# Performance work log

Hardware: AMD Instinct MI355X
Metric: run time of the kernel (lower is better)

Reference implementation:

```python
import jax, jax.numpy as jnp
import numpy as np

N, E, T = 6144, 98304, 32
D_IN, D, D_FF, H, OUT = 128, 256, 256, 4, 2
DH = D // H
EPS = 1e-5


def setup_inputs() -> dict:
    key = jax.random.key(0)
    ks = jax.random.split(key, 24)
    s = 0.05
    inp = {
        "x": jax.random.normal(ks[0], (N, D_IN), jnp.float32),
        "edge_index": jax.random.randint(ks[1], (2, E), 0, N, jnp.int64 if jax.config.jax_enable_x64 else jnp.int32),
        "timesteps": jnp.sort(jax.random.randint(ks[2], (N,), 0, T)),
        "lin_l_w": jax.random.normal(ks[3], (D, D_IN), jnp.float32) * s,
        "lin_l_b": jnp.zeros((D,), jnp.float32),
        "lin_r_w": jax.random.normal(ks[4], (D, D_IN), jnp.float32) * s,
        "bn_gamma": jnp.ones((D,), jnp.float32),
        "bn_beta": jnp.zeros((D,), jnp.float32),
        "in_proj_w": jax.random.normal(ks[5], (2, 3 * D, D), jnp.float32) * s,
        "in_proj_b": jnp.zeros((2, 3 * D), jnp.float32),
        "out_w": jax.random.normal(ks[6], (2, D, D), jnp.float32) * s,
        "out_b": jnp.zeros((2, D), jnp.float32),
        "ff1_w": jax.random.normal(ks[7], (2, D_FF, D), jnp.float32) * s,
        "ff1_b": jnp.zeros((2, D_FF), jnp.float32),
        "ff2_w": jax.random.normal(ks[8], (2, D, D_FF), jnp.float32) * s,
        "ff2_b": jnp.zeros((2, D), jnp.float32),
        "ln1_g": jnp.ones((2, D), jnp.float32),
        "ln1_b": jnp.zeros((2, D), jnp.float32),
        "ln2_g": jnp.ones((2, D), jnp.float32),
        "ln2_b": jnp.zeros((2, D), jnp.float32),
        "cls_w": jax.random.normal(ks[9], (OUT, D), jnp.float32) * s,
        "cls_b": jnp.zeros((OUT,), jnp.float32),
    }
    return inp


def _layernorm(h, g, b):
    mu = jnp.mean(h, -1, keepdims=True)
    v = jnp.var(h, -1, keepdims=True)
    return (h - mu) * jax.lax.rsqrt(v + EPS) * g + b


def _forward(x, edge_index, timesteps, lin_l_w, lin_l_b, lin_r_w, bn_gamma, bn_beta,
             in_proj_w, in_proj_b, out_w, out_b, ff1_w, ff1_b, ff2_w, ff2_b,
             ln1_g, ln1_b, ln2_g, ln2_b, cls_w, cls_b):
    # SAGEConv (mean aggregation): out = lin_l(mean_{j->i} x_j) + lin_r(x_i)
    src, dst = edge_index[0], edge_index[1]
    agg = jax.ops.segment_sum(x[src], dst, num_segments=N)
    cnt = jax.ops.segment_sum(jnp.ones((E,), x.dtype), dst, num_segments=N)
    agg = agg / jnp.maximum(cnt, 1.0)[:, None]
    h = agg @ lin_l_w.T + lin_l_b + x @ lin_r_w.T

    # BatchNorm1d (training batch stats) + ReLU
    mu = jnp.mean(h, 0)
    var = jnp.var(h, 0)
    h = (h - mu) * jax.lax.rsqrt(var + EPS) * bn_gamma + bn_beta
    h = jax.nn.relu(h)

    # Per-timestep transformer == full attention with block-diagonal mask
    mask = timesteps[:, None] == timesteps[None, :]  # [N, N]
    neg = jnp.finfo(h.dtype).min

    for l in range(2):
        # self-attention (post-norm TransformerEncoderLayer)
        qkv = h @ in_proj_w[l].T + in_proj_b[l]             # [N, 3D]
        q, k, v = jnp.split(qkv, 3, axis=-1)
        q = q.reshape(N, H, DH).transpose(1, 0, 2)          # [H, N, DH]
        k = k.reshape(N, H, DH).transpose(1, 0, 2)
        v = v.reshape(N, H, DH).transpose(1, 0, 2)
        scores = jnp.einsum('hnd,hmd->hnm', q, k) / jnp.sqrt(jnp.asarray(DH, h.dtype))
        scores = jnp.where(mask[None], scores, neg)
        attn = jax.nn.softmax(scores, axis=-1)
        o = jnp.einsum('hnm,hmd->hnd', attn, v).transpose(1, 0, 2).reshape(N, D)
        o = o @ out_w[l].T + out_b[l]
        h = _layernorm(h + o, ln1_g[l], ln1_b[l])
        # FFN
        f = jax.nn.relu(h @ ff1_w[l].T + ff1_b[l]) @ ff2_w[l].T + ff2_b[l]
        h = _layernorm(h + f, ln2_g[l], ln2_b[l])

    return h @ cls_w.T + cls_b  # [N, OUT]


def reference(x, edge_index, timesteps, lin_l_w, lin_l_b, lin_r_w, bn_gamma, bn_beta,
              in_proj_w, in_proj_b, out_w, out_b, ff1_w, ff1_b, ff2_w, ff2_b,
              ln1_g, ln1_b, ln2_g, ln2_b, cls_w, cls_b):
    return _forward(x, edge_index, timesteps, lin_l_w, lin_l_b, lin_r_w, bn_gamma, bn_beta,
                    in_proj_w, in_proj_b, out_w, out_b, ff1_w, ff1_b, ff2_w, ff2_b,
                    ln1_g, ln1_b, ln2_g, ln2_b, cls_w, cls_b)
```

## Files before the change

### kernel.cpp

```cpp
#include <hip/hip_runtime.h>

#define NN   6144
#define EE   98304
#define DIN  128
#define DD   256
#define TT   32
#define NH   4
#define ATTN_Z 6
#define WROWS 3328

typedef __attribute__((ext_vector_type(8))) short short8;
typedef __attribute__((ext_vector_type(4))) float f32x4;
typedef unsigned short u16;

__device__ __forceinline__ float bf2f(u16 u) {
    return __uint_as_float(((unsigned)u) << 16);
}
__device__ __forceinline__ u16 f2bf(float f) {
    unsigned u = __float_as_uint(f);
    return (u16)((u + 0x7fffu + ((u >> 16) & 1u)) >> 16);
}
__device__ __forceinline__ unsigned pk2(float a, float b) {
    return (unsigned)f2bf(a) | ((unsigned)f2bf(b) << 16);
}
__device__ __forceinline__ float bnrelu(float v, float s, float q, float g, float b) {
    float mu = s * (1.0f / NN);
    float var = q * (1.0f / NN) - mu * mu;
    return fmaxf((v - mu) * rsqrtf(var + 1e-5f) * g + b, 0.0f);
}

__global__ void aml_hist_k(const int* __restrict__ ei, int* __restrict__ deg) {
    int e = blockIdx.x * 256 + threadIdx.x;
    if (e < EE) atomicAdd(&deg[ei[EE + e]], 1);
}

__global__ void aml_scan_k(const int* __restrict__ deg, int* __restrict__ rowptr,
                           int* __restrict__ cursor) {
    int t = threadIdx.x;
    int base = t * 24;
    int loc[24];
    int s = 0;
    #pragma unroll
    for (int j = 0; j < 24; ++j) { loc[j] = s; s += deg[base + j]; }
    __shared__ int part[256];
    part[t] = s;
    __syncthreads();
    for (int o = 1; o < 256; o <<= 1) {
        int v = (t >= o) ? part[t - o] : 0;
        __syncthreads();
        part[t] += v;
        __syncthreads();
    }
    int off = (t > 0) ? part[t - 1] : 0;
    #pragma unroll
    for (int j = 0; j < 24; ++j) {
        rowptr[base + j] = off + loc[j];
        cursor[base + j] = off + loc[j];
    }
    if (t == 255) rowptr[NN] = part[255];
}

__global__ void aml_scatter2_k(const int* __restrict__ ei, int* __restrict__ cursor,
                               int* __restrict__ eid) {
    int e = blockIdx.x * 256 + threadIdx.x;
    if (e >= EE) return;
    int slot = atomicAdd(&cursor[ei[EE + e]], 1);
    eid[slot] = ei[e];
}

__global__ void aml_gather_k(const float* __restrict__ x, const int* __restrict__ rowptr,
                             const int* __restrict__ eid, u16* __restrict__ ac) {
    int node = blockIdx.x * 4 + (threadIdx.x >> 6);
    int lane = threadIdx.x & 63;
    int p0 = rowptr[node], p1 = rowptr[node + 1];
    float ax = 0.f, ay = 0.f;
    int j = p0;
    for (; j + 1 < p1; j += 2) {
        int s0 = eid[j], s1 = eid[j + 1];
        float2 v0 = *(const float2*)(x + (size_t)s0 * DIN + lane * 2);
        float2 v1 = *(const float2*)(x + (size_t)s1 * DIN + lane * 2);
        ax += v0.x + v1.x; ay += v0.y + v1.y;
    }
    if (j < p1) {
        float2 v = *(const float2*)(x + (size_t)eid[j] * DIN + lane * 2);
        ax += v.x; ay += v.y;
    }
    float inv = 1.0f / fmaxf((float)(p1 - p0), 1.0f);
    float2 xr = *(const float2*)(x + (size_t)node * DIN + lane * 2);
    *(unsigned*)(ac + (size_t)node * DD + lane * 2) = pk2(ax * inv, ay * inv);
    *(unsigned*)(ac + (size_t)node * DD + DIN + lane * 2) = pk2(xr.x, xr.y);
}

__global__ void aml_prep_k(const float* __restrict__ lin_l_w, const float* __restrict__ lin_r_w,
                           const float* __restrict__ inp_w, const float* __restrict__ out_w,
                           const float* __restrict__ ff1_w, const float* __restrict__ ff2_w,
                           const int* __restrict__ ts, u16* __restrict__ wb,
                           int* __restrict__ offs, float* __restrict__ zero_region) {
    int r = blockIdx.x;
    if (r > WROWS) {
        zero_region[(r - WROWS - 1) * 256 + threadIdx.x] = 0.0f;
        return;
    }
    if (r == WROWS) {
        int t = threadIdx.x;
        if (t <= TT) {
            int lo = 0, hi = NN;
            while (lo < hi) { int mid = (lo + hi) >> 1; if (ts[mid] < t) lo = mid + 1; else hi = mid; }
            offs[t] = lo;
        }
        return;
    }
    int k = threadIdx.x;
    float v;
    if (r < 256) {
        v = (k < DIN) ? lin_l_w[r * DIN + k] : lin_r_w[r * DIN + (k - DIN)];
    } else {
        int r2 = r - 256;
        int l = r2 / 1536, r3 = r2 % 1536;
        const float* src; int rr;
        if (r3 < 768)       { src = inp_w + (size_t)l * 768 * DD; rr = r3; }
        else if (r3 < 1024) { src = out_w + (size_t)l * DD * DD;  rr = r3 - 768; }
        else if (r3 < 1280) { src = ff1_w + (size_t)l * DD * DD;  rr = r3 - 1024; }
        else                { src = ff2_w + (size_t)l * DD * DD;  rr = r3 - 1280; }
        v = src[(size_t)rr * DD + k];
    }
    wb[(size_t)r * DD + k] = f2bf(v);
}

template <int RELU, int AMODE, int CF32, int BNSTAT, int CT2>
__global__ __launch_bounds__(256)
void aml_gemm_k(const void* __restrict__ A, const u16* __restrict__ Wb,
                const float* __restrict__ bias, void* __restrict__ C, int M,
                float* __restrict__ stats, const float* __restrict__ bng,
                const float* __restrict__ bnb, float* __restrict__ h2) {
    __shared__ __align__(16) unsigned char lds[65536];
    const int t = threadIdx.x;
    const int brow = blockIdx.x * 64;
    const int bcol = blockIdx.y * (64 * CT2);

    #pragma unroll
    for (int p = 0; p < 8; ++p) {
        int c = t + p * 256;
        int row = c >> 5;
        int colb = (c & 31) * 16;
        int dst = row * 512 + (colb ^ ((row & 7) << 4));
        if (AMODE == 2) {
            int d0 = (c & 31) * 8;
            const u16* sA = (const u16*)A + (size_t)(brow + row) * 256 + d0;
            uint4 raw = *(const uint4*)sA;
            const u16* rp = (const u16*)&raw;
            float av[8];
            #pragma unroll
            for (int i = 0; i < 8; ++i) {
                int d = d0 + i;
                av[i] = bnrelu(bf2f(rp[i]), stats[d], stats[DD + d], bng[d], bnb[d]);
            }
            if (blockIdx.y == 0) {
                float* hp = h2 + (size_t)(brow + row) * 256 + d0;
                *(float4*)hp = make_float4(av[0], av[1], av[2], av[3]);
                *(float4*)(hp + 4) = make_float4(av[4], av[5], av[6], av[7]);
            }
            uint4 pa = { pk2(av[0], av[1]), pk2(av[2], av[3]), pk2(av[4], av[5]), pk2(av[6], av[7]) };
            *(uint4*)(lds + dst) = pa;
        } else {
            const u16* sA = (const u16*)A + (size_t)(brow + row) * 256 + (c & 31) * 8;
            *(uint4*)(lds + dst) = *(const uint4*)sA;
        }
        *(uint4*)(lds + 32768 + dst) =
            *(const uint4*)(Wb + (size_t)(bcol + row) * 256 + (c & 31) * 8);
    }
    __syncthreads();

    const int wave = t >> 6, lane = t & 63;
    const int lrow = lane & 15, lk = lane >> 4;
    const int arow = wave * 16 + lrow;

    short8 af[8];
    #pragma unroll
    for (int ks = 0; ks < 8; ++ks) {
        int kbyte = ks * 64 + lk * 16;
        af[ks] = *(const short8*)(lds + arow * 512 + (kbyte ^ ((arow & 7) << 4)));
    }

    f32x4 acc[CT2][4] = {};
    #pragma unroll
    for (int c2 = 0; c2 < CT2; ++c2) {
        if (c2) {
            __syncthreads();
            #pragma unroll
            for (int p = 0; p < 8; ++p) {
                int c = t + p * 256;
                int row = c >> 5;
                int colb = (c & 31) * 16;
                int dst = 32768 + row * 512 + (colb ^ ((row & 7) << 4));
                *(uint4*)(lds + dst) =
                    *(const uint4*)(Wb + (size_t)(bcol + c2 * 64 + row) * 256 + (c & 31) * 8);
            }
            __syncthreads();
        }
        #pragma unroll
        for (int ks = 0; ks < 8; ++ks) {
            int kbyte = ks * 64 + lk * 16;
            #pragma unroll
            for (int ct = 0; ct < 4; ++ct) {
                int wrow = ct * 16 + lrow;
                short8 bf = *(const short8*)(lds + 32768 + wrow * 512 + (kbyte ^ ((wrow & 7) << 4)));
                acc[c2][ct] = __builtin_amdgcn_mfma_f32_16x16x32_bf16(af[ks], bf, acc[c2][ct], 0, 0, 0);
            }
        }
    }

    #pragma unroll
    for (int c2 = 0; c2 < CT2; ++c2) {
        #pragma unroll
        for (int ct = 0; ct < 4; ++ct) {
            int col = bcol + c2 * 64 + ct * 16 + lrow;
            float bv = bias[col];
            float s = 0.f, q = 0.f;
            #pragma unroll
            for (int r = 0; r < 4; ++r) {
                int grow = brow + wave * 16 + lk * 4 + r;
                float v = acc[c2][ct][r] + bv;
                if (RELU) v = fmaxf(v, 0.0f);
                if (CF32) ((float*)C)[(size_t)grow * M + col] = v;
                else      ((u16*)C)[(size_t)grow * M + col] = f2bf(v);
                if (BNSTAT) { s += v; q += v * v; }
            }
            if (BNSTAT) {
                s += __shfl_xor(s, 16); s += __shfl_xor(s, 32);
                q += __shfl_xor(q, 16); q += __shfl_xor(q, 32);
                if (lk == 0) {
                    atomicAdd(&stats[col], s);
                    atomicAdd(&stats[DD + col], q);
                }
            }
        }
    }
}

#define TAIL_GEMM(WPTR, LOADA)                                                            \
    _Pragma("unroll")                                                                     \
    for (int kc = 0; kc < 4; ++kc) {                                                      \
        __syncthreads();                                                                  \
        _Pragma("unroll")                                                                 \
        for (int p = 0; p < 8; ++p) {                                                     \
            int c = t + p * 256;                                                          \
            int row = c >> 3, sub = c & 7;                                                \
            *(uint4*)(Wl + row * 128 + ((sub * 16) ^ ((row & 7) << 4))) =                 \
                *(const uint4*)((WPTR) + (size_t)row * 256 + kc * 64 + sub * 8);          \
        }                                                                                 \
        __syncthreads();                                                                  \
        if ((LOADA) && kc == 0) {                                                         \
            _Pragma("unroll")                                                             \
            for (int ks = 0; ks < 8; ++ks) {                                              \
                int kbyte = ks * 64 + lk * 16;                                            \
                af[ks] = *(const short8*)(Al + lrow * 512 + (kbyte ^ ((lrow & 7) << 4))); \
            }                                                                             \
        }                                                                                 \
        _Pragma("unroll")                                                                 \
        for (int s = 0; s < 2; ++s) {                                                     \
            int kb = s * 64 + lk * 16;                                                    \
            _Pragma("unroll")                                                             \
            for (int ct = 0; ct < 4; ++ct) {                                              \
                int wrow = wcol + ct * 16 + lrow;                                         \
                short8 bf = *(const short8*)(Wl + wrow * 128 + (kb ^ ((wrow & 7) << 4))); \
                acc[ct] = __builtin_amdgcn_mfma_f32_16x16x32_bf16(af[kc * 2 + s], bf,     \
                                                                  acc[ct], 0, 0, 0);      \
            }                                                                             \
        }                                                                                 \
    }

#define WRITE_AL(VARR)                                                                    \
    _Pragma("unroll")                                                                     \
    for (int ct = 0; ct < 4; ++ct) {                                                      \
        _Pragma("unroll")                                                                 \
        for (int r = 0; r < 4; ++r) {                                                     \
            int row = lk * 4 + r, col = wcol + ct * 16 + lrow;                            \
            *(u16*)(Al + row * 512 + ((col * 2) ^ ((row & 7) << 4))) = f2bf(VARR[ct][r]); \
        }                                                                                 \
    }

#define ROW_LN_STATS(S4, Q4, MU, IV)                                                      \
    _Pragma("unroll")                                                                     \
    for (int off = 1; off < 16; off <<= 1) {                                              \
        _Pragma("unroll")                                                                 \
        for (int r = 0; r < 4; ++r) {                                                     \
            S4[r] += __shfl_xor(S4[r], off);                                              \
            Q4[r] += __shfl_xor(Q4[r], off);                                              \
        }                                                                                 \
    }                                                                                     \
    if (lrow == 0) {                                                                      \
        _Pragma("unroll")                                                                 \
        for (int r = 0; r < 4; ++r) {                                                     \
            reds[wave][lk * 4 + r] = S4[r];                                               \
            redq[wave][lk * 4 + r] = Q4[r];                                               \
        }                                                                                 \
    }                                                                                     \
    __syncthreads();                                                                      \
    _Pragma("unroll")                                                                     \
    for (int r = 0; r < 4; ++r) {                                                         \
        int rr = lk * 4 + r;                                                              \
        float S = reds[0][rr] + reds[1][rr] + reds[2][rr] + reds[3][rr];                  \
        float Q = redq[0][rr] + redq[1][rr] + redq[2][rr] + redq[3][rr];                  \
        MU[r] = S * (1.0f / DD);                                                          \
        IV[r] = rsqrtf(Q * (1.0f / DD) - MU[r] * MU[r] + 1e-5f);                          \
    }

template <int LAST>
__global__ __launch_bounds__(256)
void aml_tail_k(const u16* __restrict__ A, float* __restrict__ h2,
                const u16* __restrict__ Wout, const float* __restrict__ bout,
                const float* __restrict__ g1, const float* __restrict__ b1,
                const u16* __restrict__ Wff1, const float* __restrict__ bff1,
                const u16* __restrict__ Wff2, const float* __restrict__ bff2,
                const float* __restrict__ g2, const float* __restrict__ b2,
                const u16* __restrict__ Wq, const float* __restrict__ bq,
                u16* __restrict__ qkv,
                const float* __restrict__ cls_w, const float* __restrict__ cls_b,
                float* __restrict__ out) {
    __shared__ __align__(16) unsigned char Al[8192];
    __shared__ __align__(16) unsigned char Wl[32768];
    __shared__ float reds[4][16], redq[4][16];
    __shared__ float redc[2][4][16];
    const int t = threadIdx.x;
    const int brow = blockIdx.x * 16;
    const int wave = t >> 6, lane = t & 63;
    const int lrow = lane & 15, lk = lane >> 4;
    const int wcol = wave * 64;

    #pragma unroll
    for (int p = 0; p < 2; ++p) {
        int c = t + p * 256;
        int row = c >> 5, c8 = c & 31;
        *(uint4*)(Al + row * 512 + ((c8 * 16) ^ ((row & 7) << 4))) =
            *(const uint4*)(A + (size_t)(brow + row) * 256 + c8 * 8);
    }

    short8 af[8];
    f32x4 acc[4];

    #pragma unroll
    for (int ct = 0; ct < 4; ++ct) acc[ct] = (f32x4){0.f, 0.f, 0.f, 0.f};
    TAIL_GEMM(Wout, true)

    float ln1v[4][4];
    {
        float s4[4] = {}, q4[4] = {};
        #pragma unroll
        for (int ct = 0; ct < 4; ++ct) {
            int col = wcol + ct * 16 + lrow;
            float bvv = bout[col];
            #pragma unroll
            for (int r = 0; r < 4; ++r) {
                int grow = brow + lk * 4 + r;
                float v = acc[ct][r] + bvv + h2[(size_t)grow * DD + col];
                acc[ct][r] = v;
                s4[r] += v; q4[r] += v * v;
            }
        }
        float mu[4], iv[4];
        ROW_LN_STATS(s4, q4, mu, iv)
        #pragma unroll
        for (int ct = 0; ct < 4; ++ct) {
            int col = wcol + ct * 16 + lrow;
            float gv = g1[col], bb = b1[col];
            #pragma unroll
            for (int r = 0; r < 4; ++r)
                ln1v[ct][r] = (acc[ct][r] - mu[r]) * iv[r] * gv + bb;
        }
        WRITE_AL(ln1v)
    }

    #pragma unroll
    for (int ct = 0; ct < 4; ++ct) acc[ct] = (f32x4){0.f, 0.f, 0.f, 0.f};
    TAIL_GEMM(Wff1, true)
    {
        float fv[4][4];
        #pragma unroll
        for (int ct = 0; ct < 4; ++ct) {
            int col = wcol + ct * 16 + lrow;
            float bvv = bff1[col];
            #pragma unroll
            for (int r = 0; r < 4; ++r)
                fv[ct][r] = fmaxf(acc[ct][r] + bvv, 0.0f);
        }
        __syncthreads();
        WRITE_AL(fv)
    }

    #pragma unroll
    for (int ct = 0; ct < 4; ++ct) acc[ct] = (f32x4){0.f, 0.f, 0.f, 0.f};
    TAIL_GEMM(Wff2, true)
    float ln2v[4][4];
    {
        float s4[4] = {}, q4[4] = {};
        #pragma unroll
        for (int ct = 0; ct < 4; ++ct) {
            int col = wcol + ct * 16 + lrow;
            float bvv = bff2[col];
            #pragma unroll
            for (int r = 0; r < 4; ++r) {
                float v = acc[ct][r] + bvv + ln1v[ct][r];
                acc[ct][r] = v;
                s4[r] += v; q4[r] += v * v;
            }
        }
        float mu[4], iv[4];
        ROW_LN_STATS(s4, q4, mu, iv)
        #pragma unroll
        for (int ct = 0; ct < 4; ++ct) {
            int col = wcol + ct * 16 + lrow;
            float gv = g2[col], bb = b2[col];
            #pragma unroll
            for (int r = 0; r < 4; ++r) {
                float v = (acc[ct][r] - mu[r]) * iv[r] * gv + bb;
                ln2v[ct][r] = v;
                if (!LAST) {
                    int grow = brow + lk * 4 + r;
                    h2[(size_t)grow * DD + col] = v;
                }
            }
        }
        if (!LAST) {
            WRITE_AL(ln2v)
        }
    }

    if (!LAST) {
        #pragma unroll
        for (int cg = 0; cg < 3; ++cg) {
            #pragma unroll
            for (int ct = 0; ct < 4; ++ct) acc[ct] = (f32x4){0.f, 0.f, 0.f, 0.f};
            TAIL_GEMM(Wq + (size_t)cg * 256 * 256, cg == 0)
            #pragma unroll
            for (int ct = 0; ct < 4; ++ct) {
                int col = cg * 256 + wcol + ct * 16 + lrow;
                float bvv = bq[col];
                #pragma unroll
                for (int r = 0; r < 4; ++r) {
                    int grow = brow + lk * 4 + r;
                    qkv[(size_t)grow * 768 + col] = f2bf(acc[ct][r] + bvv);
                }
            }
        }
    } else {
        float c0[4] = {}, c1[4] = {};
        #pragma unroll
        for (int ct = 0; ct < 4; ++ct) {
            int col = wcol + ct * 16 + lrow;
            float w0 = cls_w[col], w1 = cls_w[DD + col];
            #pragma unroll
            for (int r = 0; r < 4; ++r) {
                c0[r] += ln2v[ct][r] * w0;
                c1[r] += ln2v[ct][r] * w1;
            }
        }
        #pragma unroll
        for (int off = 1; off < 16; off <<= 1) {
            #pragma unroll
            for (int r = 0; r < 4; ++r) {
                c0[r] += __shfl_xor(c0[r], off);
                c1[r] += __shfl_xor(c1[r], off);
            }
        }
        if (lrow == 0) {
            #pragma unroll
            for (int r = 0; r < 4; ++r) {
                redc[0][wave][lk * 4 + r] = c0[r];
                redc[1][wave][lk * 4 + r] = c1[r];
            }
        }
        __syncthreads();
        if (wave == 0 && lrow == 0) {
            float cb0 = cls_b[0], cb1 = cls_b[1];
            #pragma unroll
            for (int r = 0; r < 4; ++r) {
                int rr = lk * 4 + r;
                float o0 = redc[0][0][rr] + redc[0][1][rr] + redc[0][2][rr] + redc[0][3][rr];
                float o1 = redc[1][0][rr] + redc[1][1][rr] + redc[1][2][rr] + redc[1][3][rr];
                out[(brow + rr) * 2]     = o0 + cb0;
                out[(brow + rr) * 2 + 1] = o1 + cb1;
            }
        }
    }
}

__global__ __launch_bounds__(256)
void aml_attn_k(const u16* __restrict__ qkv, const int* __restrict__ offs,
                u16* __restrict__ o) {
    int tb = blockIdx.x, head = blockIdx.y, z = blockIdx.z;
    int start = offs[tb], end = offs[tb + 1];
    int S = end - start;
    if (S <= z * 64) return;
    int t = threadIdx.x, wave = t >> 6, lane = t & 63;
    int lq = lane & 15, lk = lane >> 4;
    int qoff = head * 64;

    __shared__ __align__(16) unsigned char Kl[8192];
    __shared__ __align__(16) unsigned char Vt[8192];
    __shared__ __align__(16) unsigned char Pl[4][2048];
    __shared__ float Ol[4][16][65];

    int qi = start + z * 64 + wave * 16 + lq;
    int qic = min(qi, end - 1);
    const u16* qp = qkv + (size_t)qic * 768 + qoff + lk * 8;
    short8 qf[2];
    qf[0] = *(const short8*)qp;
    qf[1] = *(const short8*)(qp + 32);

    float m = -1e30f, l = 0.f;
    f32x4 acc[4] = {};

    int ntile = (S + 63) >> 6;
    for (int tile = 0; tile < ntile; ++tile) {
        int jcnt = S - tile * 64; if (jcnt > 64) jcnt = 64;
        {
            int j = t >> 2, d0 = (t & 3) * 16;
            unsigned char* krow = Kl + j * 128;
            if (j < jcnt) {
                const u16* kp = qkv + (size_t)(start + tile * 64 + j) * 768 + 256 + qoff + d0;
                *(uint4*)(krow + ((d0 * 2) ^ ((j & 7) << 4))) = *(const uint4*)kp;
                *(uint4*)(krow + ((d0 * 2 + 16) ^ ((j & 7) << 4))) = *(const uint4*)(kp + 8);
            } else {
                uint4 zz = { 0, 0, 0, 0 };
                *(uint4*)(krow + ((d0 * 2) ^ ((j & 7) << 4))) = zz;
                *(uint4*)(krow + ((d0 * 2 + 16) ^ ((j & 7) << 4))) = zz;
            }
        }
        {
            int j0 = (t & 31) * 2, d0v = (t >> 5) * 8;
            const u16* vbase = qkv + (size_t)(start + tile * 64) * 768 + 512 + qoff + d0v;
            uint4 va = { 0, 0, 0, 0 }, vb = { 0, 0, 0, 0 };
            if (j0 < jcnt)     va = *(const uint4*)(vbase + (size_t)j0 * 768);
            if (j0 + 1 < jcnt) vb = *(const uint4*)(vbase + (size_t)(j0 + 1) * 768);
            const u16* pa = (const u16*)&va;
            const u16* pb = (const u16*)&vb;
            #pragma unroll
            for (int i = 0; i < 8; ++i) {
                int d = d0v + i;
                unsigned w = (unsigned)pa[i] | ((unsigned)pb[i] << 16);
                *(unsigned*)(Vt + d * 128 + ((j0 * 2) ^ ((d & 7) << 4))) = w;
            }
        }
        __syncthreads();

        f32x4 sv[4];
        #pragma unroll
        for (int kt = 0; kt < 4; ++kt) {
            int kr = kt * 16 + lq;
            f32x4 s = {};
            #pragma unroll
            for (int ks = 0; ks < 2; ++ks) {
                short8 kf = *(const short8*)(Kl + kr * 128 + ((ks * 64 + lk * 16) ^ ((kr & 7) << 4)));
                s = __builtin_amdgcn_mfma_f32_16x16x32_bf16(kf, qf[ks], s, 0, 0, 0);
            }
            sv[kt] = s;
        }
        float pm = -1e30f;
        #pragma unroll
        for (int kt = 0; kt < 4; ++kt) {
            #pragma unroll
            for (int r = 0; r < 4; ++r) {
                int kk = tile * 64 + kt * 16 + lk * 4 + r;
                float s = (kk < S) ? sv[kt][r] * 0.125f : -1e30f;
                sv[kt][r] = s;
                pm = fmaxf(pm, s);
            }
        }
        pm = fmaxf(pm, __shfl_xor(pm, 16));
        pm = fmaxf(pm, __shfl_xor(pm, 32));
        float mn = fmaxf(m, pm);
        float corr = __expf(m - mn);
        m = mn;
        float ps = 0.f;
        #pragma unroll
        for (int kt = 0; kt < 4; ++kt) {
            #pragma unroll
            for (int r = 0; r < 4; ++r) {
                float p = __expf(sv[kt][r] - mn);
                sv[kt][r] = p;
                ps += p;
            }
            uint2 w = { pk2(sv[kt][0], sv[kt][1]), pk2(sv[kt][2], sv[kt][3]) };
            *(uint2*)(Pl[wave] + lq * 128 + ((kt * 32 + lk * 8) ^ ((lq & 7) << 4))) = w;
        }
        ps += __shfl_xor(ps, 16);
        ps += __shfl_xor(ps, 32);
        l = l * corr + ps;
        #pragma unroll
        for (int dt = 0; dt < 4; ++dt) {
            #pragma unroll
            for (int r = 0; r < 4; ++r) acc[dt][r] *= corr;
        }
        #pragma unroll
        for (int ks = 0; ks < 2; ++ks) {
            short8 pf = *(const short8*)(Pl[wave] + lq * 128 + ((ks * 64 + lk * 16) ^ ((lq & 7) << 4)));
            #pragma unroll
            for (int dt = 0; dt < 4; ++dt) {
                int dr = dt * 16 + lq;
                short8 vf = *(const short8*)(Vt + dr * 128 + ((ks * 64 + lk * 16) ^ ((dr & 7) << 4)));
                acc[dt] = __builtin_amdgcn_mfma_f32_16x16x32_bf16(vf, pf, acc[dt], 0, 0, 0);
            }
        }
        __syncthreads();
    }

    float linv = 1.0f / l;
    #pragma unroll
    for (int dt = 0; dt < 4; ++dt) {
        #pragma unroll
        for (int r = 0; r < 4; ++r)
            Ol[wave][lq][dt * 16 + lk * 4 + r] = acc[dt][r] * linv;
    }
    int q2 = lane >> 2, c2 = lane & 3;
    int qg = start + z * 64 + wave * 16 + q2;
    if (qg < end) {
        u16* op = o + (size_t)qg * DD + qoff + c2 * 16;
        const float* sp = &Ol[wave][q2][c2 * 16];
        #pragma unroll
        for (int i = 0; i < 8; ++i)
            ((unsigned*)op)[i] = pk2(sp[2 * i], sp[2 * i + 1]);
    }
}

extern "C" void kernel_launch(void* const* d_in, const int* in_sizes, int n_in,
                              void* d_out, int out_size, void* d_ws, size_t ws_size,
                              hipStream_t stream) {
    const float* x       = (const float*)d_in[0];
    const int*   ei      = (const int*)d_in[1];
    const int*   ts      = (const int*)d_in[2];
    const float* lin_l_w = (const float*)d_in[3];
    const float* lin_l_b = (const float*)d_in[4];
    const float* lin_r_w = (const float*)d_in[5];
    const float* bn_g    = (const float*)d_in[6];
    const float* bn_b    = (const float*)d_in[7];
    const float* inp_w   = (const float*)d_in[8];
    const float* inp_b   = (const float*)d_in[9];
    const float* out_w   = (const float*)d_in[10];
    const float* out_b   = (const float*)d_in[11];
    const float* ff1_w   = (const float*)d_in[12];
    const float* ff1_b   = (const float*)d_in[13];
    const float* ff2_w   = (const float*)d_in[14];
    const float* ff2_b   = (const float*)d_in[15];
    const float* ln1_g   = (const float*)d_in[16];
    const float* ln1_b   = (const float*)d_in[17];
    const float* ln2_g   = (const float*)d_in[18];
    const float* ln2_b   = (const float*)d_in[19];
    const float* cls_w   = (const float*)d_in[20];
    const float* cls_b   = (const float*)d_in[21];

    float* ws     = (float*)d_ws;
    float* stats  = ws;
    int*   deg    = (int*)(stats + 512);
    int*   rowptr = deg + NN;
    int*   cursor = rowptr + NN + 4;
    int*   eid    = cursor + NN;
    int*   offs   = eid + EE;
    u16*   wb     = (u16*)(offs + 64);
    u16*   hb     = wb + (size_t)WROWS * 256;
    float* h2     = (float*)(hb + (size_t)NN * DD);
    u16*   qkv    = (u16*)(h2 + (size_t)NN * DD);
    u16*   t1     = qkv + (size_t)NN * 768;
    u16*   ac     = qkv;

    const u16* wb_cat = wb;
    const u16* wb_inp[2] = { wb + (size_t)(256) * 256,        wb + (size_t)(256 + 1536) * 256 };
    const u16* wb_out[2] = { wb + (size_t)(256 + 768) * 256,  wb + (size_t)(256 + 1536 + 768) * 256 };
    const u16* wb_ff1[2] = { wb + (size_t)(256 + 1024) * 256, wb + (size_t)(256 + 1536 + 1024) * 256 };
    const u16* wb_ff2[2] = { wb + (size_t)(256 + 1280) * 256, wb + (size_t)(256 + 1536 + 1280) * 256 };

    aml_prep_k<<<WROWS + 27, 256, 0, stream>>>(lin_l_w, lin_r_w, inp_w, out_w, ff1_w, ff2_w,
                                               ts, wb, offs, stats);
    aml_hist_k<<<EE / 256, 256, 0, stream>>>(ei, deg);
    aml_scan_k<<<1, 256, 0, stream>>>(deg, rowptr, cursor);
    aml_scatter2_k<<<EE / 256, 256, 0, stream>>>(ei, cursor, eid);
    aml_gather_k<<<NN / 4, 256, 0, stream>>>(x, rowptr, eid, ac);
    aml_gemm_k<0, 0, 0, 1, 2><<<dim3(NN / 64, 2), 256, 0, stream>>>(
        ac, wb_cat, lin_l_b, hb, DD, stats, nullptr, nullptr, nullptr);
    aml_gemm_k<0, 2, 0, 0, 2><<<dim3(NN / 64, 6), 256, 0, stream>>>(
        hb, wb_inp[0], inp_b, qkv, 768, stats, bn_g, bn_b, h2);

    aml_attn_k<<<dim3(TT, NH, ATTN_Z), 256, 0, stream>>>(qkv, offs, t1);
    aml_tail_k<0><<<NN / 16, 256, 0, stream>>>(
        t1, h2, wb_out[0], out_b, ln1_g, ln1_b,
        wb_ff1[0], ff1_b, wb_ff2[0], ff2_b, ln2_g, ln2_b,
        wb_inp[1], inp_b + 768, qkv, nullptr, nullptr, nullptr);

    aml_attn_k<<<dim3(TT, NH, ATTN_Z), 256, 0, stream>>>(qkv, offs, t1);
    aml_tail_k<1><<<NN / 16, 256, 0, stream>>>(
        t1, h2, wb_out[1], out_b + DD, ln1_g + DD, ln1_b + DD,
        wb_ff1[1], ff1_b + DD, wb_ff2[1], ff2_b + DD, ln2_g + DD, ln2_b + DD,
        nullptr, nullptr, nullptr, cls_w, cls_b, (float*)d_out);
}
```

Before: 154.8 us.

## Process two 64-query chunks per attention block to reuse staged K/V tiles

Each attention workgroup now handles 128 queries (two 64-row chunks) instead of 64. The grid z dimension is halved to match. Each K/V tile loaded into shared memory and the K fragments held in registers are reused for both chunks, halving global K/V traffic and shared-memory staging per query. The cost is more registers per thread (double accumulators and Q fragments) and fewer workgroups, which may reduce occupancy and parallelism for the small per-timestep segments.

After: 160.3 us. +3.5%, slower.

```diff
diff --git a/kernel.cpp b/kernel.cpp
--- a/kernel.cpp
+++ b/kernel.cpp
@@ -6,7 +6,7 @@
 #define DD   256
 #define TT   32
 #define NH   4
-#define ATTN_Z 6
+#define ATTN_Z 3
 #define WROWS 3328
 
 typedef __attribute__((ext_vector_type(8))) short short8;
@@ -491,7 +491,7 @@
     int tb = blockIdx.x, head = blockIdx.y, z = blockIdx.z;
     int start = offs[tb], end = offs[tb + 1];
     int S = end - start;
-    if (S <= z * 64) return;
+    if (S <= z * 128) return;
     int t = threadIdx.x, wave = t >> 6, lane = t & 63;
     int lq = lane & 15, lk = lane >> 4;
     int qoff = head * 64;
@@ -501,15 +501,18 @@
     __shared__ __align__(16) unsigned char Pl[4][2048];
     __shared__ float Ol[4][16][65];
 
-    int qi = start + z * 64 + wave * 16 + lq;
-    int qic = min(qi, end - 1);
-    const u16* qp = qkv + (size_t)qic * 768 + qoff + lk * 8;
-    short8 qf[2];
-    qf[0] = *(const short8*)qp;
-    qf[1] = *(const short8*)(qp + 32);
-
-    float m = -1e30f, l = 0.f;
-    f32x4 acc[4] = {};
+    short8 qf[2][2];
+    float m[2], l[2];
+    f32x4 acc[2][4] = {};
+    #pragma unroll
+    for (int c = 0; c < 2; ++c) {
+        int qi = start + z * 128 + c * 64 + wave * 16 + lq;
+        int qic = min(qi, end - 1);
+        const u16* qp = qkv + (size_t)qic * 768 + qoff + lk * 8;
+        qf[c][0] = *(const short8*)qp;
+        qf[c][1] = *(const short8*)(qp + 32);
+        m[c] = -1e30f; l[c] = 0.f;
+    }
 
     int ntile = (S + 63) >> 6;
     for (int tile = 0; tile < ntile; ++tile) {
@@ -544,82 +547,95 @@
         }
         __syncthreads();
 
-        f32x4 sv[4];
+        short8 kf[4][2];
         #pragma unroll
         for (int kt = 0; kt < 4; ++kt) {
             int kr = kt * 16 + lq;
-            f32x4 s = {};
+            #pragma unroll
+            for (int ks = 0; ks < 2; ++ks)
+                kf[kt][ks] = *(const short8*)(Kl + kr * 128 + ((ks * 64 + lk * 16) ^ ((kr & 7) << 4)));
+        }
+
+        #pragma unroll
+        for (int c = 0; c < 2; ++c) {
+            if (z * 128 + c * 64 >= S) break;
+            f32x4 sv[4];
+            #pragma unroll
+            for (int kt = 0; kt < 4; ++kt) {
+                f32x4 s = {};
+                s = __builtin_amdgcn_mfma_f32_16x16x32_bf16(kf[kt][0], qf[c][0], s, 0, 0, 0);
+                s = __builtin_amdgcn_mfma_f32_16x16x32_bf16(kf[kt][1], qf[c][1], s, 0, 0, 0);
+                sv[kt] = s;
+            }
+            float pm = -1e30f;
+            #pragma unroll
+            for (int kt = 0; kt < 4; ++kt) {
+                #pragma unroll
+                for (int r = 0; r < 4; ++r) {
+                    int kk = tile * 64 + kt * 16 + lk * 4 + r;
+                    float s = (kk < S) ? sv[kt][r] * 0.125f : -1e30f;
+                    sv[kt][r] = s;
+                    pm = fmaxf(pm, s);
+                }
+            }
+            pm = fmaxf(pm, __shfl_xor(pm, 16));
+            pm = fmaxf(pm, __shfl_xor(pm, 32));
+            float mn = fmaxf(m[c], pm);
+            float corr = __expf(m[c] - mn);
+            m[c] = mn;
+            float ps = 0.f;
+            #pragma unroll
+            for (int kt = 0; kt < 4; ++kt) {
+                #pragma unroll
+                for (int r = 0; r < 4; ++r) {
+                    float p = __expf(sv[kt][r] - mn);
+                    sv[kt][r] = p;
+                    ps += p;
+                }
+                uint2 w = { pk2(sv[kt][0], sv[kt][1]), pk2(sv[kt][2], sv[kt][3]) };
+                *(uint2*)(Pl[wave] + lq * 128 + ((kt * 32 + lk * 8) ^ ((lq & 7) << 4))) = w;
+            }
+            ps += __shfl_xor(ps, 16);
+            ps += __shfl_xor(ps, 32);
+            l[c] = l[c] * corr + ps;
+            #pragma unroll
+            for (int dt = 0; dt < 4; ++dt) {
+                #pragma unroll
+                for (int r = 0; r < 4; ++r) acc[c][dt][r] *= corr;
+            }
             #pragma unroll
             for (int ks = 0; ks < 2; ++ks) {
-                short8 kf = *(const short8*)(Kl + kr * 128 + ((ks * 64 + lk * 16) ^ ((kr & 7) << 4)));
-                s = __builtin_amdgcn_mfma_f32_16x16x32_bf16(kf, qf[ks], s, 0, 0, 0);
-            }
-            sv[kt] = s;
-        }
-        float pm = -1e30f;
-        #pragma unroll
-        for (int kt = 0; kt < 4; ++kt) {
-            #pragma unroll
-            for (int r = 0; r < 4; ++r) {
-                int kk = tile * 64 + kt * 16 + lk * 4 + r;
-                float s = (kk < S) ? sv[kt][r] * 0.125f : -1e30f;
-                sv[kt][r] = s;
-                pm = fmaxf(pm, s);
-            }
-        }
-        pm = fmaxf(pm, __shfl_xor(pm, 16));
-        pm = fmaxf(pm, __shfl_xor(pm, 32));
-        float mn = fmaxf(m, pm);
-        float corr = __expf(m - mn);
-        m = mn;
-        float ps = 0.f;
-        #pragma unroll
-        for (int kt = 0; kt < 4; ++kt) {
-            #pragma unroll
-            for (int r = 0; r < 4; ++r) {
-                float p = __expf(sv[kt][r] - mn);
-                sv[kt][r] = p;
-                ps += p;
-            }
-            uint2 w = { pk2(sv[kt][0], sv[kt][1]), pk2(sv[kt][2], sv[kt][3]) };
-            *(uint2*)(Pl[wave] + lq * 128 + ((kt * 32 + lk * 8) ^ ((lq & 7) << 4))) = w;
-        }
-        ps += __shfl_xor(ps, 16);
-        ps += __shfl_xor(ps, 32);
-        l = l * corr + ps;
+                short8 pf = *(const short8*)(Pl[wave] + lq * 128 + ((ks * 64 + lk * 16) ^ ((lq & 7) << 4)));
+                #pragma unroll
+                for (int dt = 0; dt < 4; ++dt) {
+                    int dr = dt * 16 + lq;
+                    short8 vf = *(const short8*)(Vt + dr * 128 + ((ks * 64 + lk * 16) ^ ((dr & 7) << 4)));
+                    acc[c][dt] = __builtin_amdgcn_mfma_f32_16x16x32_bf16(vf, pf, acc[c][dt], 0, 0, 0);
+                }
+            }
+        }
+        __syncthreads();
+    }
+
+    #pragma unroll
+    for (int c = 0; c < 2; ++c) {
+        if (z * 128 + c * 64 >= S) break;
+        float linv = 1.0f / l[c];
         #pragma unroll
         for (int dt = 0; dt < 4; ++dt) {
             #pragma unroll
-            for (int r = 0; r < 4; ++r) acc[dt][r] *= corr;
-        }
-        #pragma unroll
-        for (int ks = 0; ks < 2; ++ks) {
-            short8 pf = *(const short8*)(Pl[wave] + lq * 128 + ((ks * 64 + lk * 16) ^ ((lq & 7) << 4)));
-            #pragma unroll
-            for (int dt = 0; dt < 4; ++dt) {
-                int dr = dt * 16 + lq;
-                short8 vf = *(const short8*)(Vt + dr * 128 + ((ks * 64 + lk * 16) ^ ((dr & 7) << 4)));
-                acc[dt] = __builtin_amdgcn_mfma_f32_16x16x32_bf16(vf, pf, acc[dt], 0, 0, 0);
-            }
-        }
-        __syncthreads();
-    }
-
-    float linv = 1.0f / l;
-    #pragma unroll
-    for (int dt = 0; dt < 4; ++dt) {
-        #pragma unroll
-        for (int r = 0; r < 4; ++r)
-            Ol[wave][lq][dt * 16 + lk * 4 + r] = acc[dt][r] * linv;
-    }
-    int q2 = lane >> 2, c2 = lane & 3;
-    int qg = start + z * 64 + wave * 16 + q2;
-    if (qg < end) {
-        u16* op = o + (size_t)qg * DD + qoff + c2 * 16;
-        const float* sp = &Ol[wave][q2][c2 * 16];
-        #pragma unroll
-        for (int i = 0; i < 8; ++i)
-            ((unsigned*)op)[i] = pk2(sp[2 * i], sp[2 * i + 1]);
+            for (int r = 0; r < 4; ++r)
+                Ol[wave][lq][dt * 16 + lk * 4 + r] = acc[c][dt][r] * linv;
+        }
+        int q2 = lane >> 2, c2 = lane & 3;
+        int qg = start + z * 128 + c * 64 + wave * 16 + q2;
+        if (qg < end) {
+            u16* op = o + (size_t)qg * DD + qoff + c2 * 16;
+            const float* sp = &Ol[wave][q2][c2 * 16];
+            #pragma unroll
+            for (int i = 0; i < 8; ++i)
+                ((unsigned*)op)[i] = pk2(sp[2 * i], sp[2 * i + 1]);
+        }
     }
 }
 
```
